# Performance work log

Measured on AMD Instinct MI355X. Metric: run time of the kernel, lower is better.

## Reference

```python
import jax, jax.numpy as jnp
import numpy as np

H = 2048        # hidden_dim
D = 128         # head_dim
NQ = H // D     # 16 query heads
NKV = 4         # kv heads (GQA)
ROTARY_BASE = 10000.0


def _rope_cos_sin(seq_len, dim, dtype):
    inv_freq = 1.0 / (ROTARY_BASE ** (jnp.arange(0, dim, 2, dtype=jnp.float32) / dim))
    t = jnp.arange(seq_len, dtype=jnp.float32)
    freqs = jnp.outer(t, inv_freq)          # [S, D/2]
    return jnp.cos(freqs).astype(dtype), jnp.sin(freqs).astype(dtype)


def _apply_rope(x, cos, sin):
    # x: [B, S, H, D], non-interleaved (rotate-half) convention of flash-attn
    d2 = x.shape[-1] // 2
    x1, x2 = x[..., :d2], x[..., d2:]
    c = cos[None, :, None, :]
    s = sin[None, :, None, :]
    return jnp.concatenate([x1 * c - x2 * s, x2 * c + x1 * s], axis=-1)


def setup_inputs() -> dict:
    key = jax.random.key(0)
    ks = jax.random.split(key, 9)
    B, S = 2, 2048
    sd = 1.0 / np.sqrt(H)
    return {
        "hidden_states": jax.random.normal(ks[0], (B, S, H), jnp.float32),
        "Wq": jax.random.normal(ks[1], (H, NQ * D), jnp.float32) * sd,
        "bq": jnp.zeros((NQ * D,), jnp.float32),
        "Wk": jax.random.normal(ks[2], (H, NKV * D), jnp.float32) * sd,
        "bk": jnp.zeros((NKV * D,), jnp.float32),
        "Wv": jax.random.normal(ks[3], (H, NKV * D), jnp.float32) * sd,
        "bv": jnp.zeros((NKV * D,), jnp.float32),
        "Wc": jax.random.normal(ks[4], (NQ * D, H), jnp.float32) * sd,
        "bc": jnp.zeros((H,), jnp.float32),
    }


def reference(hidden_states, Wq, bq, Wk, bk, Wv, bv, Wc, bc):
    B, S, _ = hidden_states.shape
    scale = 1.0 / np.sqrt(D)  # scale_attn_by_inverse_layer_idx=False

    q = (hidden_states @ Wq + bq).reshape(B, S, NQ, D)
    k = (hidden_states @ Wk + bk).reshape(B, S, NKV, D)
    v = (hidden_states @ Wv + bv).reshape(B, S, NKV, D)

    cos, sin = _rope_cos_sin(S, D, q.dtype)
    q = _apply_rope(q, cos, sin)
    k = _apply_rope(k, cos, sin)

    # GQA: expand kv heads to match query heads
    rep = NQ // NKV
    k_e = jnp.repeat(k, rep, axis=2)  # [B, S, NQ, D]
    v_e = jnp.repeat(v, rep, axis=2)

    scores = jnp.einsum("bshd,bthd->bhst", q, k_e) * scale  # [B, NQ, S, S]
    causal = jnp.tril(jnp.ones((S, S), bool))
    scores = jnp.where(causal[None, None], scores, jnp.finfo(scores.dtype).min)
    probs = jax.nn.softmax(scores, axis=-1)
    attn = jnp.einsum("bhst,bthd->bshd", probs, v_e)  # [B, S, NQ, D]

    out = attn.reshape(B, S, NQ * D) @ Wc + bc  # resid dropout p=0 (eval)
    return out, k, v
```

## Files before the change

### kernel.cpp

```cpp
#include <hip/hip_runtime.h>
#include <math.h>

typedef unsigned short u16;
typedef __attribute__((ext_vector_type(8))) short s16x8;
typedef __attribute__((ext_vector_type(4))) float f32x4;
typedef __attribute__((ext_vector_type(16))) float f32x16;
typedef unsigned u32x2u __attribute__((ext_vector_type(2)));

#define B_  2
#define S_  2048
#define H_  2048
#define D_  128
#define NQ_ 16
#define NKV_ 4
#define M_  (B_*S_)
#define NQKV_ 3072

#define MFMA16(a,b,c) __builtin_amdgcn_mfma_f32_16x16x32_bf16(a,b,c,0,0,0)
#define MFMA32(a,b,c) __builtin_amdgcn_mfma_f32_32x32x16_bf16(a,b,c,0,0,0)

__device__ __forceinline__ u16 f2bf(float x) {
  union { float f; unsigned u; } v; v.f = x;
  unsigned r = v.u + 0x7fffu + ((v.u >> 16) & 1u);
  return (u16)(r >> 16);
}
__device__ __forceinline__ float bf2f(u16 x) {
  union { unsigned u; float f; } v; v.u = ((unsigned)x) << 16;
  return v.f;
}

__device__ __forceinline__ unsigned cvtpk(float lo, float hi) {
  unsigned r;
  asm("v_cvt_pk_bf16_f32 %0, %1, %2" : "=v"(r) : "v"(lo), "v"(hi));
  return r;
}

__device__ __forceinline__ void plswap(unsigned &x, unsigned &y) {
#if __has_builtin(__builtin_amdgcn_permlane32_swap)
  u32x2u r = __builtin_amdgcn_permlane32_swap(x, y, false, false);
  x = r[0]; y = r[1];
#else
  const bool hb = (threadIdx.x & 32) != 0;
  unsigned ex = (unsigned)__shfl_xor((int)x, 32, 64);
  unsigned ey = (unsigned)__shfl_xor((int)y, 32, 64);
  unsigned nx = hb ? ey : x;
  unsigned ny = hb ? y : ex;
  x = nx; y = ny;
#endif
}

__device__ __forceinline__ void gload_lds16(const u16* src, u16* dst) {
  __builtin_amdgcn_global_load_lds(
      (const __attribute__((address_space(1))) unsigned int*)src,
      (__attribute__((address_space(3))) unsigned int*)dst, 16, 0, 0);
}

__global__ __launch_bounds__(256) void cvt_x(const float* __restrict__ X, u16* __restrict__ Xb, long n4) {
  const f32x4* X4 = (const f32x4*)X;
  for (long i = (long)blockIdx.x*256 + threadIdx.x; i < n4; i += (long)gridDim.x*256) {
    f32x4 v = X4[i];
    union { u16 u[4]; unsigned long long ll; } p;
    p.u[0] = f2bf(v[0]); p.u[1] = f2bf(v[1]); p.u[2] = f2bf(v[2]); p.u[3] = f2bf(v[3]);
    ((unsigned long long*)Xb)[i] = p.ll;
  }
}

__global__ __launch_bounds__(256) void wtrans(const float* __restrict__ W, u16* __restrict__ Wt,
                                              int N, int K) {
  __shared__ float t[32][33];
  const int n0 = blockIdx.x*32, k0 = blockIdx.y*32;
  const int tx = threadIdx.x, ty = threadIdx.y;
  #pragma unroll
  for (int i = 0; i < 32; i += 8) t[ty+i][tx] = W[(long)(k0+ty+i)*N + n0 + tx];
  __syncthreads();
  #pragma unroll
  for (int i = 0; i < 32; i += 8) Wt[(long)(n0+ty+i)*K + k0 + tx] = f2bf(t[tx][ty+i]);
}

__global__ __launch_bounds__(256) void vtrans(const u16* __restrict__ QKV, u16* __restrict__ Vt) {
  __shared__ u16 t[32][33];
  const int bk = blockIdx.z;
  const int s0 = blockIdx.x*32, d0 = blockIdx.y*32;
  const int tx = threadIdx.x, ty = threadIdx.y;
  const int b = bk >> 2, kvh = bk & 3;
  #pragma unroll
  for (int i = 0; i < 32; i += 8)
    t[ty+i][tx] = QKV[(long)(b*S_ + s0+ty+i)*NQKV_ + 2560 + kvh*128 + d0 + tx];
  __syncthreads();
  #pragma unroll
  for (int i = 0; i < 32; i += 8)
    Vt[((long)bk*D_ + d0+ty+i)*S_ + s0 + tx] = t[tx][ty+i];
}

__global__ void concat_bias(const float* bq, const float* bk, const float* bv, float* bqkv) {
  int i = blockIdx.x*256 + threadIdx.x;
  if (i < NQKV_)
    bqkv[i] = (i < 2048) ? bq[i] : ((i < 2560) ? bk[i-2048] : bv[i-2560]);
}

__global__ void rope_tab(float* __restrict__ cosb, float* __restrict__ sinb) {
  int i = blockIdx.x*256 + threadIdx.x;
  int t = i >> 6, d = i & 63;
  float inv = exp2f(-(float)d * 0.20762050593045951f);
  float fr = (float)t * inv;
  float sv, cv;
  sincosf(fr, &sv, &cv);
  cosb[i] = cv; sinb[i] = sv;
}

__global__ __launch_bounds__(256) void rope_qkv(
    const u16* __restrict__ QKV, const float* __restrict__ cosb, const float* __restrict__ sinb,
    u16* __restrict__ Qb, u16* __restrict__ Kb,
    float* __restrict__ kout, float* __restrict__ vout)
{
  const float QS = 0.08838834764831845f * 1.4426950408889634f;
  const int m = blockIdx.x;
  const int b = m >> 11, s = m & 2047;
  const int tid = threadIdx.x;
  const u16* row = QKV + (long)m * NQKV_;
  const int d = tid & 63;
  const float c  = cosb[s*64 + d];
  const float sn = sinb[s*64 + d];
  #pragma unroll
  for (int i = 0; i < 4; i++) {
    int hh = (tid + i*256) >> 6;
    float x1 = bf2f(row[hh*128 + d]), x2 = bf2f(row[hh*128 + d + 64]);
    float o1 = x1*c - x2*sn, o2 = x2*c + x1*sn;
    long base = ((long)(b*NQ_ + hh)*S_ + s)*D_;
    Qb[base + d] = f2bf(o1*QS);
    Qb[base + d + 64] = f2bf(o2*QS);
  }
  {
    int kh = tid >> 6;
    float x1 = bf2f(row[2048 + kh*128 + d]), x2 = bf2f(row[2048 + kh*128 + d + 64]);
    float o1 = x1*c - x2*sn, o2 = x2*c + x1*sn;
    long kb = ((long)(b*NKV_ + kh)*S_ + s)*D_;
    Kb[kb + d] = f2bf(o1);
    Kb[kb + d + 64] = f2bf(o2);
    long ko = ((long)m*NKV_ + kh)*D_;
    kout[ko + d] = o1;
    kout[ko + d + 64] = o2;
  }
  #pragma unroll
  for (int i = 0; i < 2; i++) {
    int e = tid + i*256;
    vout[(long)m*512 + e] = bf2f(row[2560 + e]);
  }
}

template<int BM, int BN, int WN, typename OutT>
__global__ __launch_bounds__(512, 2) void gemm8p(
    const u16* __restrict__ A, const u16* __restrict__ Bm,
    const float* __restrict__ bias, OutT* __restrict__ C,
    int M, int N, int K)
{
  constexpr int WM  = 8 / WN;
  constexpr int RW  = (BM/2) / WM;
  constexpr int JA  = RW / 16;
  constexpr int CW  = (BN/2) / WN;
  constexpr int JB  = CW / 16;
  constexpr int ALD = BM/128;
  constexpr int BLD = BN/128;
  constexpr int VMC = ALD + BLD;
  __shared__ u16 As[2][BM*64];
  __shared__ u16 Bs[2][BN*64];

  const int tid = threadIdx.x;
  const int lane = tid & 63, w = tid >> 6;
  const int r16 = lane & 15, g = lane >> 4;
  const int wrn = w / WN, wcn = w % WN;

  const int gx = gridDim.x;
  const int nwg = gx * gridDim.y;
  const int id = blockIdx.y * gx + blockIdx.x;
  const int cpx = nwg >> 3;
  const int sid = (id & 7) * cpx + (id >> 3);
  const long m0 = (long)(sid / gx) * BM;
  const long n0 = (long)(sid % gx) * BN;

  const u16* Ag = A + m0 * K;
  const u16* Bg = Bm + n0 * K;

  auto stageA = [&](int buf, int h, int k0) {
    #pragma unroll
    for (int i = 0; i < ALD; i++) {
      const int slot = i*512 + tid;
      const int row = h*(BM/2) + (slot >> 3), cg = slot & 7;
      const u16* src = Ag + (long)row*K + k0 + ((cg ^ (row & 7)) * 8);
      gload_lds16(src, &As[buf][h*(BM*32) + slot*8]);
    }
  };
  auto stageB = [&](int buf, int h, int k0) {
    #pragma unroll
    for (int i = 0; i < BLD; i++) {
      const int slot = i*512 + tid;
      const int row = h*(BN/2) + (slot >> 3), cg = slot & 7;
      const u16* src = Bg + (long)row*K + k0 + ((cg ^ (row & 7)) * 8);
      gload_lds16(src, &Bs[buf][h*(BN*32) + slot*8]);
    }
  };

  f32x4 acc[2*JA][2*JB] = {};
  s16x8 Ar[JA][2], Br[JB][2];
  const int nt = K >> 6;

#define PHASE(BUF, MH, NH, RDA, RDB, STMT)                                        \
  do {                                                                            \
    if (RDA) {                                                                    \
      _Pragma("unroll") for (int j = 0; j < JA; j++)                              \
        _Pragma("unroll") for (int kk = 0; kk < 2; kk++) {                        \
          const int R = (MH)*(BM/2) + wrn*RW + j*16 + r16;                        \
          Ar[j][kk] = *(const s16x8*)&As[BUF][R*64 + (((kk*4 + g) ^ (R & 7))*8)]; \
        }                                                                         \
    }                                                                             \
    if (RDB) {                                                                    \
      _Pragma("unroll") for (int jj = 0; jj < JB; jj++)                           \
        _Pragma("unroll") for (int kk = 0; kk < 2; kk++) {                        \
          const int Cc = (NH)*(BN/2) + wcn*CW + jj*16 + r16;                      \
          Br[jj][kk] = *(const s16x8*)&Bs[BUF][Cc*64 + (((kk*4 + g) ^ (Cc & 7))*8)]; \
        }                                                                         \
    }                                                                             \
    STMT;                                                                         \
    __builtin_amdgcn_s_barrier();                                                 \
    asm volatile("s_waitcnt lgkmcnt(0)" ::: "memory");                            \
    __builtin_amdgcn_sched_barrier(0);                                            \
    __builtin_amdgcn_s_setprio(1);                                                \
    _Pragma("unroll") for (int j = 0; j < JA; j++)                                \
      _Pragma("unroll") for (int jj = 0; jj < JB; jj++)                           \
        _Pragma("unroll") for (int kk = 0; kk < 2; kk++)                          \
          acc[(MH)*JA + j][(NH)*JB + jj] =                                        \
            MFMA16(Ar[j][kk], Br[jj][kk], acc[(MH)*JA + j][(NH)*JB + jj]);        \
    __builtin_amdgcn_s_setprio(0);                                                \
    __builtin_amdgcn_s_barrier();                                                 \
  } while (0)

  stageA(0, 0, 0); stageA(0, 1, 0); stageB(0, 0, 0); stageB(0, 1, 0);
  if (nt > 1) { stageA(1, 0, 64); stageB(1, 1, 64); }

  for (int t = 0; t < nt; t++) {
    const int X = t & 1, Y = X ^ 1;
    if (t == nt - 1) {
      asm volatile("s_waitcnt vmcnt(0)" ::: "memory");
    } else if constexpr (VMC == 4) {
      asm volatile("s_waitcnt vmcnt(4)" ::: "memory");
    } else {
      asm volatile("s_waitcnt vmcnt(3)" ::: "memory");
    }
    __builtin_amdgcn_s_barrier();
    PHASE(X, 0, 0, true,  true,  { if (t+1 < nt) stageA(Y, 1, (t+1)*64); });
    PHASE(X, 0, 1, false, true,  { if (t+1 < nt) stageB(Y, 0, (t+1)*64); });
    PHASE(X, 1, 1, true,  false, { if (t+2 < nt) stageA(X, 0, (t+2)*64); });
    PHASE(X, 1, 0, false, true,  { if (t+2 < nt) stageB(X, 1, (t+2)*64); });
  }
#undef PHASE

  #pragma unroll
  for (int mh = 0; mh < 2; mh++)
    #pragma unroll
    for (int j = 0; j < JA; j++)
      #pragma unroll
      for (int nh = 0; nh < 2; nh++)
        #pragma unroll
        for (int jj = 0; jj < JB; jj++) {
          const int col = nh*(BN/2) + wcn*CW + jj*16 + r16;
          const float bv = bias[n0 + col];
          #pragma unroll
          for (int r = 0; r < 4; r++) {
            const long row = m0 + mh*(BM/2) + wrn*RW + j*16 + g*4 + r;
            const float vv = acc[mh*JA + j][nh*JB + jj][r] + bv;
            if constexpr (sizeof(OutT) == 2)
              C[row * N + n0 + col] = (OutT)f2bf(vv);
            else
              C[row * N + n0 + col] = (OutT)vv;
          }
        }
}

__global__ __launch_bounds__(256, 2) void attn_kernel(
    const u16* __restrict__ Qb, const u16* __restrict__ Kb,
    const u16* __restrict__ Vt, u16* __restrict__ Ob)
{
  __shared__ u16 Ks[2][64*128];
  __shared__ u16 Vs[2][64*128];
  const int tid = threadIdx.x;
  const int lane = tid & 63, w = tid >> 6;
  const int l31 = lane & 31, hi = lane >> 5;
  const int id = blockIdx.x;
  const int bh = id & 31;
  const int b = bh >> 4, h = bh & 15;
  const int p = id >> 5;
  const int qt = (p < 8) ? (15 - p) : (p - 8);
  const int kvh = h >> 2;
  const int q0w = qt*128 + w*32;
  const int nt = 2*qt + 2;

  const u16* Qg = Qb + (((long)(b*NQ_ + h))*S_ + q0w)*D_;
  const u16* Kg = Kb + ((long)(b*NKV_ + kvh))*S_*D_;
  const u16* Vg = Vt + ((long)(b*NKV_ + kvh))*D_*S_;

  s16x8 qf[8];
  #pragma unroll
  for (int ks = 0; ks < 8; ks++)
    qf[ks] = *(const s16x8*)&Qg[l31*D_ + ks*16 + hi*8];

  f32x16 po[4] = {};
  float mrow = -1e30f, lrow = 0.f;

  auto stage = [&](int buf, int kv0s) {
    #pragma unroll
    for (int i = 0; i < 4; i++) {
      const int c = i*4 + w;
      const int G = c*64 + lane;
      const int krow = G >> 4, kcg = G & 15;
      const u16* gk = Kg + (long)(kv0s + krow)*D_ + ((kcg ^ (krow & 15)) * 8);
      gload_lds16(gk, &Ks[buf][c*512]);
      const int o = c*512 + lane*8;
      const int d2 = o >> 7, t16 = (o >> 3) & 15;
      const int gidx = t16 ^ (d2 & 15);
      const int dsr = ((gidx >> 3) << 6) + d2;
      const u16* gv = Vg + (long)dsr*S_ + kv0s + ((gidx & 7) * 8);
      gload_lds16(gv, &Vs[buf][c*512]);
    }
  };

  auto compute = [&](int buf, int t) {
    const int kv0 = t*64;
    if (kv0 > q0w + 31) return;
    f32x16 sc[2] = {};
    __builtin_amdgcn_s_setprio(1);
    #pragma unroll
    for (int ks = 0; ks < 8; ks++) {
      #pragma unroll
      for (int ct = 0; ct < 2; ct++) {
        const int row = ct*32 + l31;
        s16x8 kf = *(const s16x8*)&Ks[buf][row*128 + ((ks*16 + hi*8) ^ ((row & 15)*8))];
        sc[ct] = MFMA32(kf, qf[ks], sc[ct]);
      }
    }
    __builtin_amdgcn_s_setprio(0);
    if (kv0 + 63 > q0w) {
      const int qrow = q0w + l31;
      #pragma unroll
      for (int ct = 0; ct < 2; ct++)
        #pragma unroll
        for (int r = 0; r < 16; r++) {
          int kv = kv0 + ct*32 + (r & 3) + 8*(r >> 2) + 4*hi;
          if (kv > qrow) sc[ct][r] = -3.0e38f;
        }
    }
    float pm = sc[0][0];
    #pragma unroll
    for (int ct = 0; ct < 2; ct++)
      #pragma unroll
      for (int r = 0; r < 16; r++) pm = fmaxf(pm, sc[ct][r]);
    pm = fmaxf(pm, __shfl_xor(pm, 32, 64));
    if (!__all(pm - mrow <= 8.0f)) {
      float mn = fmaxf(mrow, pm);
      float fr = exp2f(mrow - mn);
      mrow = mn;
      lrow *= fr;
      #pragma unroll
      for (int r = 0; r < 16; r++) {
        float frv = __shfl(fr, (r & 3) + 8*(r >> 2) + 4*hi, 64);
        #pragma unroll
        for (int dt = 0; dt < 4; dt++) po[dt][r] *= frv;
      }
    }
    float ps = 0.f;
    #pragma unroll
    for (int ct = 0; ct < 2; ct++)
      #pragma unroll
      for (int r = 0; r < 16; r++) {
        float pv = exp2f(sc[ct][r] - mrow);
        sc[ct][r] = pv;
        ps += pv;
      }
    ps += __shfl_xor(ps, 32, 64);
    lrow += ps;
    unsigned mw[2][8];
    #pragma unroll
    for (int ct = 0; ct < 2; ct++)
      #pragma unroll
      for (int wd = 0; wd < 8; wd++)
        mw[ct][wd] = cvtpk(sc[ct][2*wd], sc[ct][2*wd + 1]);
    s16x8 pa[4];
    #pragma unroll
    for (int ct = 0; ct < 2; ct++)
      #pragma unroll
      for (int pp = 0; pp < 2; pp++) {
        unsigned a0 = mw[ct][4*pp + 0], b0 = mw[ct][4*pp + 2];
        unsigned a1 = mw[ct][4*pp + 1], b1 = mw[ct][4*pp + 3];
        plswap(a0, b0);
        plswap(a1, b1);
        union { unsigned u[4]; s16x8 v; } pu;
        pu.u[0] = a0; pu.u[1] = a1; pu.u[2] = b0; pu.u[3] = b1;
        pa[ct*2 + pp] = pu.v;
      }
    __builtin_amdgcn_s_setprio(1);
    #pragma unroll
    for (int ks2 = 0; ks2 < 4; ks2++)
      #pragma unroll
      for (int dt = 0; dt < 4; dt++) {
        const int d = dt*32 + l31, d2 = d & 63;
        const int gidx = ((d >> 6) << 3) + ks2*2 + hi;
        s16x8 vf = *(const s16x8*)&Vs[buf][d2*128 + ((gidx ^ (d2 & 15)) * 8)];
        po[dt] = MFMA32(pa[ks2], vf, po[dt]);
      }
    __builtin_amdgcn_s_setprio(0);
  };

  stage(0, 0);
  for (int t = 0; t < nt; t += 2) {
    stage(1, (t + 1)*64);
    asm volatile("s_waitcnt vmcnt(8)" ::: "memory");
    __builtin_amdgcn_s_barrier();
    compute(0, t);
    __builtin_amdgcn_s_barrier();
    if (t + 2 < nt) {
      stage(0, (t + 2)*64);
      asm volatile("s_waitcnt vmcnt(8)" ::: "memory");
    } else {
      asm volatile("s_waitcnt vmcnt(0)" ::: "memory");
    }
    __builtin_amdgcn_s_barrier();
    compute(1, t + 1);
    __builtin_amdgcn_s_barrier();
  }

  float inv = 1.0f / lrow;
  #pragma unroll
  for (int r = 0; r < 16; r++) {
    const int qr = (r & 3) + 8*(r >> 2) + 4*hi;
    float invq = __shfl(inv, qr, 64);
    const long q = (long)q0w + qr;
    #pragma unroll
    for (int dt = 0; dt < 4; dt++)
      Ob[((long)b*S_ + q)*H_ + h*D_ + dt*32 + l31] = f2bf(po[dt][r]*invq);
  }
}

extern "C" void kernel_launch(void* const* d_in, const int* in_sizes, int n_in,
                              void* d_out, int out_size, void* d_ws, size_t ws_size,
                              hipStream_t stream) {
  const float* hs = (const float*)d_in[0];
  const float* Wq = (const float*)d_in[1];
  const float* bq = (const float*)d_in[2];
  const float* Wk = (const float*)d_in[3];
  const float* bk = (const float*)d_in[4];
  const float* Wv = (const float*)d_in[5];
  const float* bv = (const float*)d_in[6];
  const float* Wc = (const float*)d_in[7];
  const float* bc = (const float*)d_in[8];

  float* out  = (float*)d_out;
  float* kout = out + (long)M_*H_;
  float* vout = kout + (long)M_*NKV_*D_;

  char* ws = (char*)d_ws;
  u16*  Xbf   = (u16*)ws;
  u16*  Wqkvt = Xbf + (long)M_*H_;
  u16*  Wct   = Wqkvt + (long)NQKV_*H_;
  float* bqkv = (float*)(Wct + (long)H_*H_);
  u16*  QKV   = (u16*)(bqkv + NQKV_);
  float* cosb = (float*)(QKV + (long)M_*NQKV_);
  float* sinb = cosb + S_*64;
  u16*  Qbf   = (u16*)(sinb + S_*64);
  u16*  Kbf   = Qbf + (long)B_*NQ_*S_*D_;
  u16*  Vtb   = Kbf + (long)B_*NKV_*S_*D_;
  u16*  Obf   = Vtb + (long)B_*NKV_*D_*S_;

  cvt_x<<<2048, 256, 0, stream>>>(hs, Xbf, (long)M_*H_/4);
  wtrans<<<dim3(64,64), dim3(32,8), 0, stream>>>(Wq, Wqkvt, 2048, 2048);
  wtrans<<<dim3(16,64), dim3(32,8), 0, stream>>>(Wk, Wqkvt + 2048L*2048, 512, 2048);
  wtrans<<<dim3(16,64), dim3(32,8), 0, stream>>>(Wv, Wqkvt + 2560L*2048, 512, 2048);
  wtrans<<<dim3(64,64), dim3(32,8), 0, stream>>>(Wc, Wct, 2048, 2048);
  concat_bias<<<12, 256, 0, stream>>>(bq, bk, bv, bqkv);
  rope_tab<<<512, 256, 0, stream>>>(cosb, sinb);

  gemm8p<128, 384, 4, u16><<<dim3(NQKV_/384, M_/128), 512, 0, stream>>>(
      Xbf, Wqkvt, bqkv, QKV, M_, NQKV_, H_);
  rope_qkv<<<M_, 256, 0, stream>>>(QKV, cosb, sinb, Qbf, Kbf, kout, vout);
  vtrans<<<dim3(S_/32, D_/32, B_*NKV_), dim3(32,8), 0, stream>>>(QKV, Vtb);
  attn_kernel<<<dim3(512), 256, 0, stream>>>(Qbf, Kbf, Vtb, Obf);
  gemm8p<256, 128, 2, float><<<dim3(H_/128, M_/256), 512, 0, stream>>>(
      Obf, Wct, bc, out, M_, H_, H_);
}
```

Measured before the change: 212.4 us.

## Drop attention K/V double buffering to single buffer for higher occupancy

Replaces the double-buffered K/V LDS pipeline in the attention kernel with a single buffer: load a tile, wait for all loads, barrier, compute, barrier. LDS per block halves from 64KB to 32KB, and launch bounds rise to 4 blocks per CU, so the intent is to hide latency through occupancy rather than in-block prefetch. The cost is that load latency is no longer overlapped within a block, and the tighter register budget may cause spills given the large accumulator state.

```diff
diff --git a/kernel.cpp b/kernel.cpp
--- a/kernel.cpp
+++ b/kernel.cpp
@@ -276,12 +276,12 @@
         }
 }
 
-__global__ __launch_bounds__(256, 2) void attn_kernel(
+__global__ __launch_bounds__(256, 4) void attn_kernel(
     const u16* __restrict__ Qb, const u16* __restrict__ Kb,
     const u16* __restrict__ Vt, u16* __restrict__ Ob)
 {
-  __shared__ u16 Ks[2][64*128];
-  __shared__ u16 Vs[2][64*128];
+  __shared__ u16 Ks[64*128];
+  __shared__ u16 Vs[64*128];
   const int tid = threadIdx.x;
   const int lane = tid & 63, w = tid >> 6;
   const int l31 = lane & 31, hi = lane >> 5;
@@ -306,124 +306,108 @@
   f32x16 po[4] = {};
   float mrow = -1e30f, lrow = 0.f;
 
-  auto stage = [&](int buf, int kv0s) {
+  for (int t = 0; t < nt; t++) {
+    const int kv0 = t*64;
     #pragma unroll
     for (int i = 0; i < 4; i++) {
       const int c = i*4 + w;
       const int G = c*64 + lane;
       const int krow = G >> 4, kcg = G & 15;
-      const u16* gk = Kg + (long)(kv0s + krow)*D_ + ((kcg ^ (krow & 15)) * 8);
-      gload_lds16(gk, &Ks[buf][c*512]);
+      const u16* gk = Kg + (long)(kv0 + krow)*D_ + ((kcg ^ (krow & 15)) * 8);
+      gload_lds16(gk, &Ks[c*512]);
       const int o = c*512 + lane*8;
       const int d2 = o >> 7, t16 = (o >> 3) & 15;
       const int gidx = t16 ^ (d2 & 15);
       const int dsr = ((gidx >> 3) << 6) + d2;
-      const u16* gv = Vg + (long)dsr*S_ + kv0s + ((gidx & 7) * 8);
-      gload_lds16(gv, &Vs[buf][c*512]);
+      const u16* gv = Vg + (long)dsr*S_ + kv0 + ((gidx & 7) * 8);
+      gload_lds16(gv, &Vs[c*512]);
     }
-  };
-
-  auto compute = [&](int buf, int t) {
-    const int kv0 = t*64;
-    if (kv0 > q0w + 31) return;
-    f32x16 sc[2] = {};
-    __builtin_amdgcn_s_setprio(1);
-    #pragma unroll
-    for (int ks = 0; ks < 8; ks++) {
-      #pragma unroll
-      for (int ct = 0; ct < 2; ct++) {
-        const int row = ct*32 + l31;
-        s16x8 kf = *(const s16x8*)&Ks[buf][row*128 + ((ks*16 + hi*8) ^ ((row & 15)*8))];
-        sc[ct] = MFMA32(kf, qf[ks], sc[ct]);
+    asm volatile("s_waitcnt vmcnt(0)" ::: "memory");
+    __builtin_amdgcn_s_barrier();
+
+    if (kv0 <= q0w + 31) {
+      f32x16 sc[2] = {};
+      __builtin_amdgcn_s_setprio(1);
+      #pragma unroll
+      for (int ks = 0; ks < 8; ks++) {
+        #pragma unroll
+        for (int ct = 0; ct < 2; ct++) {
+          const int row = ct*32 + l31;
+          s16x8 kf = *(const s16x8*)&Ks[row*128 + ((ks*16 + hi*8) ^ ((row & 15)*8))];
+          sc[ct] = MFMA32(kf, qf[ks], sc[ct]);
+        }
       }
+      __builtin_amdgcn_s_setprio(0);
+      if (kv0 + 63 > q0w) {
+        const int qrow = q0w + l31;
+        #pragma unroll
+        for (int ct = 0; ct < 2; ct++)
+          #pragma unroll
+          for (int r = 0; r < 16; r++) {
+            int kv = kv0 + ct*32 + (r & 3) + 8*(r >> 2) + 4*hi;
+            if (kv > qrow) sc[ct][r] = -3.0e38f;
+          }
+      }
+      float pm = sc[0][0];
+      #pragma unroll
+      for (int ct = 0; ct < 2; ct++)
+        #pragma unroll
+        for (int r = 0; r < 16; r++) pm = fmaxf(pm, sc[ct][r]);
+      pm = fmaxf(pm, __shfl_xor(pm, 32, 64));
+      if (!__all(pm - mrow <= 8.0f)) {
+        float mn = fmaxf(mrow, pm);
+        float fr = exp2f(mrow - mn);
+        mrow = mn;
+        lrow *= fr;
+        #pragma unroll
+        for (int r = 0; r < 16; r++) {
+          float frv = __shfl(fr, (r & 3) + 8*(r >> 2) + 4*hi, 64);
+          #pragma unroll
+          for (int dt = 0; dt < 4; dt++) po[dt][r] *= frv;
+        }
+      }
+      float ps = 0.f;
+      #pragma unroll
+      for (int ct = 0; ct < 2; ct++)
+        #pragma unroll
+        for (int r = 0; r < 16; r++) {
+          float pv = exp2f(sc[ct][r] - mrow);
+          sc[ct][r] = pv;
+          ps += pv;
+        }
+      ps += __shfl_xor(ps, 32, 64);
+      lrow += ps;
+      unsigned mw[2][8];
+      #pragma unroll
+      for (int ct = 0; ct < 2; ct++)
+        #pragma unroll
+        for (int wd = 0; wd < 8; wd++)
+          mw[ct][wd] = cvtpk(sc[ct][2*wd], sc[ct][2*wd + 1]);
+      s16x8 pa[4];
+      #pragma unroll
+      for (int ct = 0; ct < 2; ct++)
+        #pragma unroll
+        for (int pp = 0; pp < 2; pp++) {
+          unsigned a0 = mw[ct][4*pp + 0], b0 = mw[ct][4*pp + 2];
+          unsigned a1 = mw[ct][4*pp + 1], b1 = mw[ct][4*pp + 3];
+          plswap(a0, b0);
+          plswap(a1, b1);
+          union { unsigned u[4]; s16x8 v; } pu;
+          pu.u[0] = a0; pu.u[1] = a1; pu.u[2] = b0; pu.u[3] = b1;
+          pa[ct*2 + pp] = pu.v;
+        }
+      __builtin_amdgcn_s_setprio(1);
+      #pragma unroll
+      for (int ks2 = 0; ks2 < 4; ks2++)
+        #pragma unroll
+        for (int dt = 0; dt < 4; dt++) {
+          const int d = dt*32 + l31, d2 = d & 63;
+          const int gidx = ((d >> 6) << 3) + ks2*2 + hi;
+          s16x8 vf = *(const s16x8*)&Vs[d2*128 + ((gidx ^ (d2 & 15)) * 8)];
+          po[dt] = MFMA32(pa[ks2], vf, po[dt]);
+        }
+      __builtin_amdgcn_s_setprio(0);
     }
-    __builtin_amdgcn_s_setprio(0);
-    if (kv0 + 63 > q0w) {
-      const int qrow = q0w + l31;
-      #pragma unroll
-      for (int ct = 0; ct < 2; ct++)
-        #pragma unroll
-        for (int r = 0; r < 16; r++) {
-          int kv = kv0 + ct*32 + (r & 3) + 8*(r >> 2) + 4*hi;
-          if (kv > qrow) sc[ct][r] = -3.0e38f;
-        }
-    }
-    float pm = sc[0][0];
-    #pragma unroll
-    for (int ct = 0; ct < 2; ct++)
-      #pragma unroll
-      for (int r = 0; r < 16; r++) pm = fmaxf(pm, sc[ct][r]);
-    pm = fmaxf(pm, __shfl_xor(pm, 32, 64));
-    if (!__all(pm - mrow <= 8.0f)) {
-      float mn = fmaxf(mrow, pm);
-      float fr = exp2f(mrow - mn);
-      mrow = mn;
-      lrow *= fr;
-      #pragma unroll
-      for (int r = 0; r < 16; r++) {
-        float frv = __shfl(fr, (r & 3) + 8*(r >> 2) + 4*hi, 64);
-        #pragma unroll
-        for (int dt = 0; dt < 4; dt++) po[dt][r] *= frv;
-      }
-    }
-    float ps = 0.f;
-    #pragma unroll
-    for (int ct = 0; ct < 2; ct++)
-      #pragma unroll
-      for (int r = 0; r < 16; r++) {
-        float pv = exp2f(sc[ct][r] - mrow);
-        sc[ct][r] = pv;
-        ps += pv;
-      }
-    ps += __shfl_xor(ps, 32, 64);
-    lrow += ps;
-    unsigned mw[2][8];
-    #pragma unroll
-    for (int ct = 0; ct < 2; ct++)
-      #pragma unroll
-      for (int wd = 0; wd < 8; wd++)
-        mw[ct][wd] = cvtpk(sc[ct][2*wd], sc[ct][2*wd + 1]);
-    s16x8 pa[4];
-    #pragma unroll
-    for (int ct = 0; ct < 2; ct++)
-      #pragma unroll
-      for (int pp = 0; pp < 2; pp++) {
-        unsigned a0 = mw[ct][4*pp + 0], b0 = mw[ct][4*pp + 2];
-        unsigned a1 = mw[ct][4*pp + 1], b1 = mw[ct][4*pp + 3];
-        plswap(a0, b0);
-        plswap(a1, b1);
-        union { unsigned u[4]; s16x8 v; } pu;
-        pu.u[0] = a0; pu.u[1] = a1; pu.u[2] = b0; pu.u[3] = b1;
-        pa[ct*2 + pp] = pu.v;
-      }
-    __builtin_amdgcn_s_setprio(1);
-    #pragma unroll
-    for (int ks2 = 0; ks2 < 4; ks2++)
-      #pragma unroll
-      for (int dt = 0; dt < 4; dt++) {
-        const int d = dt*32 + l31, d2 = d & 63;
-        const int gidx = ((d >> 6) << 3) + ks2*2 + hi;
-        s16x8 vf = *(const s16x8*)&Vs[buf][d2*128 + ((gidx ^ (d2 & 15)) * 8)];
-        po[dt] = MFMA32(pa[ks2], vf, po[dt]);
-      }
-    __builtin_amdgcn_s_setprio(0);
-  };
-
-  stage(0, 0);
-  for (int t = 0; t < nt; t += 2) {
-    stage(1, (t + 1)*64);
-    asm volatile("s_waitcnt vmcnt(8)" ::: "memory");
-    __builtin_amdgcn_s_barrier();
-    compute(0, t);
-    __builtin_amdgcn_s_barrier();
-    if (t + 2 < nt) {
-      stage(0, (t + 2)*64);
-      asm volatile("s_waitcnt vmcnt(8)" ::: "memory");
-    } else {
-      asm volatile("s_waitcnt vmcnt(0)" ::: "memory");
-    }
-    __builtin_amdgcn_s_barrier();
-    compute(1, t + 1);
     __builtin_amdgcn_s_barrier();
   }
 
```

Result: slower. 387.0 us (+82.2%).
